# Kernel tuning notes

Hardware: AMD Instinct MI355X
Metric: run time of the kernel (lower is better)

The kernel has to match this reference:

```python
import jax, jax.numpy as jnp
import numpy as np

B, P, D, F = 2048, 16, 1024, 512  # batch, n_prompt, dim, fusion_dim
S = 2 * P  # sequence length
H = D // 2  # classifier hidden
LN_EPS = 1e-5


def _ln_relu(y, g, b):
    mu = jnp.mean(y, axis=-1, keepdims=True)
    var = jnp.mean(jnp.square(y - mu), axis=-1, keepdims=True)
    return jax.nn.relu((y - mu) * jax.lax.rsqrt(var + LN_EPS) * g + b)


def setup_inputs() -> dict:
    key = jax.random.key(0)
    ks = jax.random.split(key, 24)
    n = lambda k, shp, scale: jax.random.normal(k, shp, dtype=jnp.float32) * scale
    return {
        "q": n(ks[0], (B, S, D), 1.0),
        # nn.MultiheadAttention (1 head, batch_first)
        "in_proj_w": n(ks[1], (3 * D, D), 1.0 / np.sqrt(D)),
        "in_proj_b": jnp.zeros((3 * D,), jnp.float32),
        "out_w": n(ks[2], (D, D), 1.0 / np.sqrt(D)),
        "out_b": jnp.zeros((D,), jnp.float32),
        # 32 per-position classifiers, stacked: Linear(D,H)+ReLU+Linear(H,1)+ReLU
        "cls_w1": n(ks[3], (S, H, D), 1.0 / np.sqrt(D)),
        "cls_b1": jnp.zeros((S, H), jnp.float32),
        "cls_w2": n(ks[4], (S, H), 1.0 / np.sqrt(H)),
        "cls_b2": jnp.zeros((S,), jnp.float32),
        # fusion / projector heads: Linear(D,F)+LayerNorm(F)+ReLU
        "fus_w": n(ks[5], (F, D), 1.0 / np.sqrt(D)),
        "fus_b": jnp.zeros((F,), jnp.float32),
        "fus_g": jnp.ones((F,), jnp.float32),
        "fus_be": jnp.zeros((F,), jnp.float32),
        "pa_w": n(ks[6], (F, D), 1.0 / np.sqrt(D)),
        "pa_b": jnp.zeros((F,), jnp.float32),
        "pa_g": jnp.ones((F,), jnp.float32),
        "pa_be": jnp.zeros((F,), jnp.float32),
        "pv_w": n(ks[7], (F, D), 1.0 / np.sqrt(D)),
        "pv_b": jnp.zeros((F,), jnp.float32),
        "pv_g": jnp.ones((F,), jnp.float32),
        "pv_be": jnp.zeros((F,), jnp.float32),
    }


def reference(q, in_proj_w, in_proj_b, out_w, out_b,
              cls_w1, cls_b1, cls_w2, cls_b2,
              fus_w, fus_b, fus_g, fus_be,
              pa_w, pa_b, pa_g, pa_be,
              pv_w, pv_b, pv_g, pv_be):
    # --- single-head self-attention (nn.MultiheadAttention, eval mode) ---
    wq, wk, wv = jnp.split(in_proj_w, 3, axis=0)
    bq, bk, bv = jnp.split(in_proj_b, 3, axis=0)
    qp = jnp.einsum('bsd,ed->bse', q, wq) + bq
    kp = jnp.einsum('bsd,ed->bse', q, wk) + bk
    vp = jnp.einsum('bsd,ed->bse', q, wv) + bv
    scores = jnp.einsum('bse,bte->bst', qp, kp) / jnp.sqrt(jnp.float32(D))
    attn = jax.nn.softmax(scores, axis=-1)
    q_att = jnp.einsum('bst,bte->bse', attn, vp)
    q_att = jnp.einsum('bse,de->bsd', q_att, out_w) + out_b

    # --- per-position tiny classifiers, batched over the 32 slots ---
    h = jax.nn.relu(jnp.einsum('bsd,shd->bsh', q, cls_w1) + cls_b1)  # [B,S,H]
    d = jax.nn.relu(jnp.einsum('bsh,sh->bs', h, cls_w2) + cls_b2)    # [B,S]

    d_a = jax.nn.softmax(d[:, :P], axis=-1)
    d_v = jax.nn.softmax(d[:, P:], axis=-1)
    audio = jnp.einsum('bsd,bs->bd', q_att[:, :P, :], d_a)
    video = jnp.einsum('bsd,bs->bd', q_att[:, P:, :], d_v)
    fusion = (audio + video) * 0.5

    fusion_h = _ln_relu(fusion @ fus_w.T + fus_b, fus_g, fus_be)
    fusion_a = _ln_relu(audio @ pa_w.T + pa_b, pa_g, pa_be)
    fusion_v = _ln_relu(video @ pv_w.T + pv_b, pv_g, pv_be)
    return (fusion_h, fusion_a, fusion_v, d_a, d_v)
```

## Files before the change

### kernel.cpp

```cpp
#include <hip/hip_runtime.h>

#define Bdim 2048
#define Sdim 32
#define Ddim 1024
#define Fdim 512
#define Hdim 512

typedef __bf16 bf16_t;
typedef __bf16 bf16x8 __attribute__((ext_vector_type(8)));
typedef __bf16 bf16x4 __attribute__((ext_vector_type(4)));
typedef float  f32x4  __attribute__((ext_vector_type(4)));

#define BM 128
#define BN 128
#define BK 32

__device__ __forceinline__ void gll16(const bf16_t* g, bf16_t* l) {
  __builtin_amdgcn_global_load_lds((const __attribute__((address_space(1))) void*)g,
                                   (__attribute__((address_space(3))) void*)l,
                                   16, 0, 0);
}

__device__ __forceinline__ int swz32(int row, int k) {
  return row * 32 + (((((k >> 3) ^ ((row >> 1) & 3))) << 3) | (k & 7));
}

__global__ void k_cvt_all(const float* __restrict__ q, const float* __restrict__ ipw,
                          const float* __restrict__ ow, const float* __restrict__ cw1,
                          const float* __restrict__ fusw, const float* __restrict__ paw,
                          const float* __restrict__ pvw,
                          bf16_t* __restrict__ q16, bf16_t* __restrict__ w16,
                          bf16_t* __restrict__ ow16, bf16_t* __restrict__ cls16,
                          bf16_t* __restrict__ hw16) {
  long v = (long)blockIdx.x * 256 + threadIdx.x;
  const float* s; bf16_t* d; long off;
  if (v < 16777216L)      { s = q;    d = q16;            off = 0; }
  else if (v < 17563648L) { s = ipw;  d = w16;            off = 16777216L; }
  else if (v < 17825792L) { s = ow;   d = ow16;           off = 17563648L; }
  else if (v < 22020096L) { s = cw1;  d = cls16;          off = 17825792L; }
  else if (v < 22151168L) { s = fusw; d = hw16;           off = 22020096L; }
  else if (v < 22282240L) { s = paw;  d = hw16 + 524288;  off = 22151168L; }
  else                    { s = pvw;  d = hw16 + 1048576; off = 22282240L; }
  long i = (v - off) * 4;
  float4 t = *(const float4*)(s + i);
  bf16x4 o;
  o[0] = (bf16_t)t.x; o[1] = (bf16_t)t.y; o[2] = (bf16_t)t.z; o[3] = (bf16_t)t.w;
  *(bf16x4*)(d + i) = o;
}

__global__ void k_bias_pre(const float* __restrict__ ipw, const float* __restrict__ ipb,
                           const float* __restrict__ ow, const float* __restrict__ ob,
                           float* __restrict__ u, float* __restrict__ w,
                           float* __restrict__ bp, float* __restrict__ c0) {
  int blk = blockIdx.x, tid = threadIdx.x;
  if (blk < 4) {
    int d = blk * 256 + tid;
    float acc = 0.f;
    #pragma unroll 8
    for (int e = 0; e < Ddim; ++e) acc += ipw[(long)e * Ddim + d] * ipb[Ddim + e];
    u[d] = acc;
  } else if (blk < 8) {
    int d = (blk - 4) * 256 + tid;
    float acc = 0.f;
    #pragma unroll 8
    for (int e = 0; e < Ddim; ++e) acc += ipw[(long)(Ddim + e) * Ddim + d] * ipb[e];
    w[d] = acc;
  } else if (blk < 136) {
    int o = (blk - 8) * 8 + (tid >> 5);
    int l = tid & 31;
    float acc = 0.f;
    #pragma unroll 4
    for (int e = l; e < Ddim; e += 32) acc += ow[(long)o * Ddim + e] * ipb[2 * Ddim + e];
    #pragma unroll
    for (int m = 1; m < 32; m <<= 1) acc += __shfl_xor(acc, m);
    if (l == 0) bp[o] = acc + ob[o];
  } else {
    __shared__ float red[256];
    float acc = 0.f;
    for (int e = tid; e < Ddim; e += 256) acc += ipb[e] * ipb[Ddim + e];
    red[tid] = acc;
    __syncthreads();
    for (int off = 128; off; off >>= 1) {
      if (tid < off) red[tid] += red[tid + off];
      __syncthreads();
    }
    if (tid == 0) c0[0] = red[0];
  }
}

template<int AT, int BT>
__device__ __forceinline__ void gemm_tile(const bf16_t* __restrict__ A, long lda,
                                          const bf16_t* __restrict__ Bt, long ldb,
                                          long m0, long n0, int K,
                                          bf16_t* sa, bf16_t* sb, f32x4 acc[4][4]) {
  const int tid  = threadIdx.x;
  const int wave = tid >> 6;
  const int lane = tid & 63;
  const int quad = lane >> 4;
  const int l16  = lane & 15;
  const int wm = (wave & 1) * 64;
  const int wn = (wave >> 1) * 64;

  for (int kt = 0; kt < K; kt += BK) {
    __syncthreads();
    if constexpr (AT == 0) {
      #pragma unroll
      for (int r = 0; r < 2; ++r) {
        int L = r * 256 + tid;
        int row = L >> 2, cs = L & 3;
        int csrc = cs ^ ((row >> 1) & 3);
        gll16(A + (m0 + row) * lda + kt + csrc * 8, sa + (long)(r * 256 + wave * 64) * 8);
      }
    } else {
      #pragma unroll
      for (int r = 0; r < 2; ++r) {
        int L = r * 256 + tid;
        int gk = L >> 4, gm = (L & 15) * 8;
        bf16x8 v = *(const bf16x8*)(A + (long)(kt + gk) * lda + m0 + gm);
        #pragma unroll
        for (int j = 0; j < 8; ++j) sa[swz32(gm + j, gk)] = v[j];
      }
    }
    if constexpr (BT == 0) {
      #pragma unroll
      for (int r = 0; r < 2; ++r) {
        int L = r * 256 + tid;
        int row = L >> 2, cs = L & 3;
        int csrc = cs ^ ((row >> 1) & 3);
        gll16(Bt + (n0 + row) * ldb + kt + csrc * 8, sb + (long)(r * 256 + wave * 64) * 8);
      }
    } else {
      #pragma unroll
      for (int r = 0; r < 2; ++r) {
        int L = r * 256 + tid;
        int gk = L >> 4, gn = (L & 15) * 8;
        bf16x8 v = *(const bf16x8*)(Bt + (long)(kt + gk) * ldb + n0 + gn);
        #pragma unroll
        for (int j = 0; j < 8; ++j) sb[swz32(gn + j, gk)] = v[j];
      }
    }
    __syncthreads();
    bf16x8 af[4], bfr[4];
    #pragma unroll
    for (int i = 0; i < 4; ++i) {
      int row = wm + i * 16 + l16;
      af[i] = *(const bf16x8*)(sa + row * 32 + ((quad ^ ((row >> 1) & 3)) << 3));
    }
    #pragma unroll
    for (int j = 0; j < 4; ++j) {
      int row = wn + j * 16 + l16;
      bfr[j] = *(const bf16x8*)(sb + row * 32 + ((quad ^ ((row >> 1) & 3)) << 3));
    }
    #pragma unroll
    for (int i = 0; i < 4; ++i)
      #pragma unroll
      for (int j = 0; j < 4; ++j)
        acc[i][j] = __builtin_amdgcn_mfma_f32_16x16x32_bf16(bfr[j], af[i], acc[i][j], 0, 0, 0);
  }
}

template<int AT, int BT>
__global__ __launch_bounds__(256) void k_gemm_bf16(
    const bf16_t* __restrict__ A, long lda, long sAz,
    const bf16_t* __restrict__ Bt, long ldb, long sBz,
    bf16_t* __restrict__ C, long ldc, long sCz,
    const float* __restrict__ bias, int K) {
  __shared__ bf16_t sa[BM * BK];
  __shared__ bf16_t sb[BN * BK];
  long n0 = (long)blockIdx.x * BN;
  long m0 = (long)blockIdx.y * BM;
  long z  = blockIdx.z;
  const bf16_t* Az = A + z * sAz;
  const bf16_t* Bz = Bt + z * sBz;
  bf16_t* Cz = C + z * sCz;
  f32x4 acc[4][4];
  #pragma unroll
  for (int i = 0; i < 4; ++i)
    #pragma unroll
    for (int j = 0; j < 4; ++j) acc[i][j] = (f32x4){0.f, 0.f, 0.f, 0.f};
  gemm_tile<AT, BT>(Az, lda, Bz, ldb, m0, n0, K, sa, sb, acc);
  const int tid = threadIdx.x, wave = tid >> 6, lane = tid & 63;
  const int quad = lane >> 4, l16 = lane & 15;
  const int wm = (wave & 1) * 64, wn = (wave >> 1) * 64;
  #pragma unroll
  for (int i = 0; i < 4; ++i) {
    long row = m0 + wm + i * 16 + l16;
    #pragma unroll
    for (int j = 0; j < 4; ++j) {
      long col = n0 + wn + j * 16 + quad * 4;
      f32x4 b4 = bias ? *(const f32x4*)(bias + col) : (f32x4){0.f, 0.f, 0.f, 0.f};
      bf16x4 o;
      #pragma unroll
      for (int r = 0; r < 4; ++r) o[r] = (bf16_t)(acc[i][j][r] + b4[r]);
      *(bf16x4*)(Cz + row * ldc + col) = o;
    }
  }
}

__global__ __launch_bounds__(256) void k_gemm_f32(
    const bf16_t* __restrict__ A, long lda, long sAz,
    const bf16_t* __restrict__ Bt, long ldb, long sBz,
    float* __restrict__ C, long ldc, long sCz, int K) {
  __shared__ bf16_t sa[BM * BK];
  __shared__ bf16_t sb[BN * BK];
  long n0 = (long)blockIdx.x * BN;
  long m0 = (long)blockIdx.y * BM;
  long z  = blockIdx.z;
  const bf16_t* Az = A + z * sAz;
  const bf16_t* Bz = Bt + z * sBz;
  float* Cz = C + z * sCz;
  f32x4 acc[4][4];
  #pragma unroll
  for (int i = 0; i < 4; ++i)
    #pragma unroll
    for (int j = 0; j < 4; ++j) acc[i][j] = (f32x4){0.f, 0.f, 0.f, 0.f};
  gemm_tile<0, 0>(Az, lda, Bz, ldb, m0, n0, K, sa, sb, acc);
  const int tid = threadIdx.x, wave = tid >> 6, lane = tid & 63;
  const int quad = lane >> 4, l16 = lane & 15;
  const int wm = (wave & 1) * 64, wn = (wave >> 1) * 64;
  #pragma unroll
  for (int i = 0; i < 4; ++i) {
    long row = m0 + wm + i * 16 + l16;
    #pragma unroll
    for (int j = 0; j < 4; ++j) {
      long col = n0 + wn + j * 16 + quad * 4;
      *(f32x4*)(Cz + row * ldc + col) = acc[i][j];
    }
  }
}

__global__ __launch_bounds__(512, 2) void k_gemm_big8(
    const bf16_t* __restrict__ A, const bf16_t* __restrict__ Bt,
    bf16_t* __restrict__ C) {
  __shared__ bf16_t sa[2][256 * 64];
  __shared__ bf16_t sb[2][256 * 64];
  const int tid = threadIdx.x, wave = tid >> 6, lane = tid & 63;
  const int quad = lane >> 4, l16 = lane & 15;
  int lin = blockIdx.x;
  int c = lin & 7, t0 = lin >> 3;
  int wg = c * 128 + t0;
  long m0 = (long)(wg >> 2) * 256;
  long n0 = (long)(wg & 3) * 256;
  const int wm = (wave >> 2) * 128;
  const int wn = (wave & 3) * 64;

  const int csA = tid & 7;
  const bf16_t* aSrc = A + (m0 + (tid >> 3)) * 1024 + (long)((csA ^ ((tid >> 4) & 7)) * 8);
  const int t2 = tid & 255;
  const bf16_t* bSrc = Bt + (n0 + (t2 >> 3)) * 1024 + (long)(((t2 & 7) ^ ((t2 >> 4) & 7)) * 8);

  const int swzk0 = ((0 * 4 + quad) ^ (l16 >> 1)) << 3;
  const int swzk1 = ((1 * 4 + quad) ^ (l16 >> 1)) << 3;
  const int aBase = (wm + l16) * 64;
  const int bBase = (wn + l16) * 64;

  f32x4 acc[8][4];
  #pragma unroll
  for (int i = 0; i < 8; ++i)
    #pragma unroll
    for (int j = 0; j < 4; ++j) acc[i][j] = (f32x4){0.f, 0.f, 0.f, 0.f};

  bf16x8 afc[8], bfr0[4], bfr1[4];

#define ST_AQ(SB, KT, Q) \
  gll16(aSrc + (long)(Q) * 65536 + (KT), &sa[SB][(Q) * 4096 + wave * 512])
#define ST_BP(SB, KT, OA, OB) do {                                             \
    int oct_ = (wave < 4) ? (OA) : (OB);                                       \
    gll16(bSrc + (long)oct_ * 32768 + (KT),                                    \
          &sb[SB][oct_ * 2048 + (wave & 3) * 512]);                            \
  } while (0)

#define LD_AF(CB, MH) do {                                                     \
    _Pragma("unroll")                                                          \
    for (int i = 0; i < 4; ++i) {                                              \
      afc[i * 2 + 0] = *(const bf16x8*)(&sa[CB][aBase + (MH) * 4096 + i * 1024 + swzk0]); \
      afc[i * 2 + 1] = *(const bf16x8*)(&sa[CB][aBase + (MH) * 4096 + i * 1024 + swzk1]); \
    } } while (0)
#define LD_BF(CB, NH, DST) do {                                                \
    _Pragma("unroll")                                                          \
    for (int jj = 0; jj < 2; ++jj) {                                           \
      DST[jj * 2 + 0] = *(const bf16x8*)(&sb[CB][bBase + (NH) * 2048 + jj * 1024 + swzk0]); \
      DST[jj * 2 + 1] = *(const bf16x8*)(&sb[CB][bBase + (NH) * 2048 + jj * 1024 + swzk1]); \
    } } while (0)

#define MFMA16(BF, IOFF, JOFF) do {                                            \
    __builtin_amdgcn_s_setprio(1);                                             \
    _Pragma("unroll")                                                          \
    for (int i = 0; i < 4; ++i)                                                \
      _Pragma("unroll")                                                        \
      for (int jj = 0; jj < 2; ++jj)                                           \
        _Pragma("unroll")                                                      \
        for (int kh = 0; kh < 2; ++kh)                                         \
          acc[(IOFF) + i][(JOFF) + jj] = __builtin_amdgcn_mfma_f32_16x16x32_bf16( \
              BF[jj * 2 + kh], afc[i * 2 + kh], acc[(IOFF) + i][(JOFF) + jj], 0, 0, 0); \
    __builtin_amdgcn_s_setprio(0);                                             \
    __builtin_amdgcn_sched_barrier(0);                                         \
  } while (0)

#define BAR1() do {                                                            \
    asm volatile("" ::: "memory");                                             \
    __builtin_amdgcn_s_barrier();                                              \
    asm volatile("s_waitcnt lgkmcnt(0)" ::: "memory");                         \
    __builtin_amdgcn_sched_barrier(0);                                         \
  } while (0)
#define BAR2V() do {                                                           \
    asm volatile("s_waitcnt vmcnt(4)" ::: "memory");                           \
    __builtin_amdgcn_s_barrier();                                              \
    asm volatile("" ::: "memory");                                             \
  } while (0)
#define BAR2() do {                                                            \
    asm volatile("" ::: "memory");                                             \
    __builtin_amdgcn_s_barrier();                                              \
    asm volatile("" ::: "memory");                                             \
  } while (0)

#define TILE(CB, SB, KT2) do {                                                 \
                                                    \
    LD_AF(CB, 0); LD_BF(CB, 0, bfr0);                                          \
    ST_AQ(SB, KT2, 0); ST_AQ(SB, KT2, 2);                                      \
    BAR1(); MFMA16(bfr0, 0, 0); BAR2V();                                       \
                                                    \
    LD_BF(CB, 1, bfr1);                                                        \
    ST_BP(SB, KT2, 0, 4); ST_BP(SB, KT2, 2, 6);                                \
    BAR1(); MFMA16(bfr1, 0, 2); BAR2V();                                       \
                                                    \
    LD_AF(CB, 1);                                                              \
    ST_BP(SB, KT2, 1, 5); ST_BP(SB, KT2, 3, 7);                                \
    BAR1(); MFMA16(bfr1, 4, 2); BAR2();                                        \
              \
    ST_AQ(SB, KT2, 1); ST_AQ(SB, KT2, 3);                                      \
    BAR1(); MFMA16(bfr0, 4, 0); BAR2V();                                       \
  } while (0)

  ST_AQ(0, 0, 0); ST_AQ(0, 0, 2);
  ST_BP(0, 0, 0, 4); ST_BP(0, 0, 2, 6);
  ST_BP(0, 0, 1, 5); ST_BP(0, 0, 3, 7);
  ST_AQ(0, 0, 1); ST_AQ(0, 0, 3);
  BAR2V();

  #pragma unroll 1
  for (int x = 0; x < 16; x += 2) {
    int ktA = (x + 1) * 64;
    int ktB = (x + 2) * 64;
    TILE(0, 1, ktA);
    TILE(1, 0, ktB);
  }

#undef ST_AQ
#undef ST_BP
#undef LD_AF
#undef LD_BF
#undef MFMA16
#undef BAR1
#undef BAR2V
#undef BAR2
#undef TILE

  #pragma unroll
  for (int i = 0; i < 8; ++i) {
    long row = m0 + wm + i * 16 + l16;
    #pragma unroll
    for (int j = 0; j < 4; ++j) {
      long col = n0 + wn + j * 16 + quad * 4;
      bf16x4 o;
      #pragma unroll
      for (int r = 0; r < 4; ++r) o[r] = (bf16_t)(acc[i][j][r]);
      *(bf16x4*)(C + row * 1024 + col) = o;
    }
  }
}

__global__ __launch_bounds__(256) void k_gemm_cls(
    const bf16_t* __restrict__ q16, const bf16_t* __restrict__ w1,
    const float* __restrict__ b1, const float* __restrict__ w2,
    float* __restrict__ dsum) {
  __shared__ bf16_t sa[BM * BK];
  __shared__ bf16_t sb[BN * BK];
  int lin = ((int)blockIdx.z * 16 + blockIdx.y) * 4 + blockIdx.x;
  int c = lin & 7, j0 = lin >> 3;
  int p = c + 8 * (j0 >> 2);
  long n0 = (long)(j0 & 3) * BN;
  int s = p >> 4;
  long m0 = (long)(p & 15) * BM;
  const bf16_t* A  = q16 + (long)s * Ddim;
  const bf16_t* Bt = w1 + (long)s * Hdim * Ddim;
  f32x4 acc[4][4];
  #pragma unroll
  for (int i = 0; i < 4; ++i)
    #pragma unroll
    for (int j = 0; j < 4; ++j) acc[i][j] = (f32x4){0.f, 0.f, 0.f, 0.f};
  gemm_tile<0, 0>(A, (long)Sdim * Ddim, Bt, Ddim, m0, n0, Ddim, sa, sb, acc);
  const int tid = threadIdx.x, wave = tid >> 6, lane = tid & 63;
  const int quad = lane >> 4, l16 = lane & 15;
  const int wm = (wave & 1) * 64, wn = (wave >> 1) * 64;
  const float* b1s = b1 + (long)s * Hdim;
  const float* w2s = w2 + (long)s * Hdim;
  #pragma unroll
  for (int i = 0; i < 4; ++i) {
    float vsum = 0.f;
    #pragma unroll
    for (int j = 0; j < 4; ++j) {
      long col = n0 + wn + j * 16 + quad * 4;
      f32x4 b4 = *(const f32x4*)(b1s + col);
      f32x4 w4 = *(const f32x4*)(w2s + col);
      #pragma unroll
      for (int r = 0; r < 4; ++r)
        vsum += fmaxf(acc[i][j][r] + b4[r], 0.f) * w4[r];
    }
    vsum += __shfl_xor(vsum, 16);
    vsum += __shfl_xor(vsum, 32);
    if (lane < 16) {
      long row = m0 + wm + i * 16 + l16;
      atomicAdd(&dsum[row * Sdim + s], vsum);
    }
  }
}

__global__ void k_finalize_d(const float* __restrict__ dsum, const float* __restrict__ cb2,
                             float* __restrict__ daws, float* __restrict__ out_da,
                             float* __restrict__ out_dv) {
  int t = blockIdx.x * 256 + threadIdx.x;
  int b = t >> 5, s = t & 31;
  float v = fmaxf(dsum[t] + cb2[s], 0.f);
  float m = v;
  #pragma unroll
  for (int mask = 1; mask < 16; mask <<= 1) m = fmaxf(m, __shfl_xor(m, mask));
  float e = __expf(v - m);
  float sum = e;
  #pragma unroll
  for (int mask = 1; mask < 16; mask <<= 1) sum += __shfl_xor(sum, mask);
  float r = e / sum;
  daws[t] = r;
  if (s < 16) out_da[b * 16 + s] = r;
  else        out_dv[b * 16 + (s - 16)] = r;
}

#define QPAD 264
__global__ __launch_bounds__(256) void k_attn_pool(
    const bf16_t* __restrict__ q16, const bf16_t* __restrict__ G16,
    const float* __restrict__ daws, const float* __restrict__ u,
    const float* __restrict__ wv, const float* __restrict__ c0p,
    bf16_t* __restrict__ pooled) {
  __shared__ bf16_t qc[32 * QPAD];
  __shared__ bf16_t gc[32 * QPAD];
  __shared__ float sc[32][33];
  __shared__ float qup[32][8], qwp[32][8];
  __shared__ float quL[32], qwL[32], caL[32], cvL[32], daL[16], dvL[16];
  const int tid = threadIdx.x, wave = tid >> 6, lane = tid & 63;
  const int quad = lane >> 4, l16 = lane & 15;
  const long b = blockIdx.x;
  const bf16_t* qb = q16 + b * (Sdim * Ddim);
  const bf16_t* gb = G16 + b * (Sdim * Ddim);
  if (tid < 32) {
    float dval = daws[b * Sdim + tid];
    if (tid < 16) daL[tid] = dval; else dvL[tid - 16] = dval;
  }
  qup[tid >> 3][tid & 7] = 0.f;
  qwp[tid >> 3][tid & 7] = 0.f;
  const int ti = wave & 1, tj = wave >> 1;
  f32x4 acc = (f32x4){0.f, 0.f, 0.f, 0.f};
  for (int kc = 0; kc < Ddim; kc += 256) {
    __syncthreads();
    #pragma unroll
    for (int r = 0; r < 4; ++r) {
      int L = r * 256 + tid;
      int row = L >> 5, koff = (L & 31) * 8;
      *(bf16x8*)(qc + row * QPAD + koff) = *(const bf16x8*)(qb + (long)row * Ddim + kc + koff);
      *(bf16x8*)(gc + row * QPAD + koff) = *(const bf16x8*)(gb + (long)row * Ddim + kc + koff);
    }
    __syncthreads();
    #pragma unroll
    for (int kk = 0; kk < 8; ++kk) {
      bf16x8 a  = *(const bf16x8*)(gc + (ti * 16 + l16) * QPAD + kk * 32 + quad * 8);
      bf16x8 bb = *(const bf16x8*)(qc + (tj * 16 + l16) * QPAD + kk * 32 + quad * 8);
      acc = __builtin_amdgcn_mfma_f32_16x16x32_bf16(a, bb, acc, 0, 0, 0);
    }
    {
      int s2 = tid & 31, sl = tid >> 5;
      float pu = 0.f, pw = 0.f;
      const bf16_t* qrow = qc + s2 * QPAD + sl * 32;
      const float* ub = u + kc + sl * 32;
      const float* wb = wv + kc + sl * 32;
      #pragma unroll
      for (int kb = 0; kb < 4; ++kb) {
        bf16x8 qv = *(const bf16x8*)(qrow + kb * 8);
        f32x4 u0 = *(const f32x4*)(ub + kb * 8);
        f32x4 u1 = *(const f32x4*)(ub + kb * 8 + 4);
        f32x4 w0 = *(const f32x4*)(wb + kb * 8);
        f32x4 w1 = *(const f32x4*)(wb + kb * 8 + 4);
        #pragma unroll
        for (int e = 0; e < 4; ++e) {
          pu += (float)qv[e] * u0[e] + (float)qv[e + 4] * u1[e];
          pw += (float)qv[e] * w0[e] + (float)qv[e + 4] * w1[e];
        }
      }
      qup[s2][sl] += pu;
      qwp[s2][sl] += pw;
    }
  }
  __syncthreads();
  if (tid < 32) {
    float a0 = 0.f, a1 = 0.f;
    for (int k = 0; k < 8; ++k) { a0 += qup[tid][k]; a1 += qwp[tid][k]; }
    quL[tid] = a0; qwL[tid] = a1;
  }
  __syncthreads();
  {
    float c00 = c0p[0];
    int col = tj * 16 + l16;
    #pragma unroll
    for (int r = 0; r < 4; ++r) {
      int row = ti * 16 + quad * 4 + r;
      sc[row][col] = (acc[r] + quL[row] + qwL[col] + c00) * 0.03125f;
    }
  }
  __syncthreads();
  if (tid < 32) {
    float mx = -1e30f;
    for (int t = 0; t < 32; ++t) mx = fmaxf(mx, sc[tid][t]);
    float sum = 0.f;
    for (int t = 0; t < 32; ++t) { float e = __expf(sc[tid][t] - mx); sc[tid][t] = e; sum += e; }
    float inv = 1.f / sum;
    for (int t = 0; t < 32; ++t) sc[tid][t] *= inv;
  }
  __syncthreads();
  if (tid < 32) {
    float a0 = 0.f, a1 = 0.f;
    for (int s2 = 0; s2 < 16; ++s2) a0 += daL[s2] * sc[s2][tid];
    for (int s2 = 0; s2 < 16; ++s2) a1 += dvL[s2] * sc[16 + s2][tid];
    caL[tid] = a0; cvL[tid] = a1;
  }
  __syncthreads();
  {
    int d0 = tid * 4;
    float ap[4] = {0.f, 0.f, 0.f, 0.f}, vp[4] = {0.f, 0.f, 0.f, 0.f};
    for (int t = 0; t < 32; ++t) {
      float ca = caL[t], cv = cvL[t];
      bf16x4 qv = *(const bf16x4*)(qb + (long)t * Ddim + d0);
      #pragma unroll
      for (int e = 0; e < 4; ++e) {
        float x = (float)qv[e];
        ap[e] += ca * x;
        vp[e] += cv * x;
      }
    }
    bf16x4 pf, pa, pv;
    #pragma unroll
    for (int e = 0; e < 4; ++e) {
      pf[e] = (bf16_t)(0.5f * (ap[e] + vp[e]));
      pa[e] = (bf16_t)ap[e];
      pv[e] = (bf16_t)vp[e];
    }
    *(bf16x4*)(pooled + b * 3072 + d0)        = pf;
    *(bf16x4*)(pooled + b * 3072 + 1024 + d0) = pa;
    *(bf16x4*)(pooled + b * 3072 + 2048 + d0) = pv;
  }
}

__global__ __launch_bounds__(256) void k_ln(
    const float* __restrict__ Y,
    const float* __restrict__ fb, const float* __restrict__ fg, const float* __restrict__ fbe,
    const float* __restrict__ ab, const float* __restrict__ ag, const float* __restrict__ abe,
    const float* __restrict__ vb, const float* __restrict__ vg, const float* __restrict__ vbe,
    float* __restrict__ out) {
  int wave = threadIdx.x >> 6, lane = threadIdx.x & 63;
  long row = (long)blockIdx.x * 4 + wave;
  int head = (int)(row >> 11);
  const float* bb = (head == 0) ? fb : (head == 1) ? ab : vb;
  const float* gg = (head == 0) ? fg : (head == 1) ? ag : vg;
  const float* be = (head == 0) ? fbe : (head == 1) ? abe : vbe;
  const float* y = Y + row * Fdim + lane * 8;
  float v[8];
  float s = 0.f;
  #pragma unroll
  for (int k = 0; k < 8; ++k) { v[k] = y[k] + bb[lane * 8 + k]; s += v[k]; }
  #pragma unroll
  for (int m = 1; m < 64; m <<= 1) s += __shfl_xor(s, m);
  float mu = s * (1.f / Fdim);
  float vs = 0.f;
  #pragma unroll
  for (int k = 0; k < 8; ++k) { float t = v[k] - mu; vs += t * t; }
  #pragma unroll
  for (int m = 1; m < 64; m <<= 1) vs += __shfl_xor(vs, m);
  float inv = rsqrtf(vs * (1.f / Fdim) + 1e-5f);
  float* o = out + row * Fdim + lane * 8;
  #pragma unroll
  for (int k = 0; k < 8; ++k) {
    float t = (v[k] - mu) * inv * gg[lane * 8 + k] + be[lane * 8 + k];
    o[k] = fmaxf(t, 0.f);
  }
}

extern "C" void kernel_launch(void* const* d_in, const int* in_sizes, int n_in,
                              void* d_out, int out_size, void* d_ws, size_t ws_size,
                              hipStream_t stream) {
  const float* q    = (const float*)d_in[0];
  const float* ipw  = (const float*)d_in[1];
  const float* ipb  = (const float*)d_in[2];
  const float* ow   = (const float*)d_in[3];
  const float* ob   = (const float*)d_in[4];
  const float* cw1  = (const float*)d_in[5];
  const float* cb1  = (const float*)d_in[6];
  const float* cw2  = (const float*)d_in[7];
  const float* cb2  = (const float*)d_in[8];
  const float* fusw = (const float*)d_in[9];
  const float* fusb = (const float*)d_in[10];
  const float* fusg = (const float*)d_in[11];
  const float* fusbe= (const float*)d_in[12];
  const float* paw  = (const float*)d_in[13];
  const float* pab  = (const float*)d_in[14];
  const float* pag  = (const float*)d_in[15];
  const float* pabe = (const float*)d_in[16];
  const float* pvw  = (const float*)d_in[17];
  const float* pvb  = (const float*)d_in[18];
  const float* pvg  = (const float*)d_in[19];
  const float* pvbe = (const float*)d_in[20];
  float* out = (float*)d_out;

  const size_t o_q16   = 0;
  const size_t o_w16   = 134217728;
  const size_t o_ow16  = 140509184;
  const size_t o_cls16 = 142606336;
  const size_t o_hw16  = 176160768;
  const size_t o_Mt    = 179306496;
  const size_t o_Nt    = 181403648;
  const size_t o_G16   = 183500800;
  const size_t o_pool  = 317718528;
  const size_t o_u     = 330301440;
  const size_t o_wv    = 330305536;
  const size_t o_bp    = 330309632;
  const size_t o_c0    = 330313728;
  const size_t o_dsum  = 330313984;
  const size_t o_daws  = 330576128;
  const size_t total   = 330838272;
  if (ws_size < total) return;

  char* ws = (char*)d_ws;
  bf16_t* q16   = (bf16_t*)(ws + o_q16);
  bf16_t* w16   = (bf16_t*)(ws + o_w16);
  bf16_t* Wq16  = w16;
  bf16_t* Wk16  = w16 + 1048576;
  bf16_t* Wv16  = w16 + 2097152;
  bf16_t* ow16  = (bf16_t*)(ws + o_ow16);
  bf16_t* cls16 = (bf16_t*)(ws + o_cls16);
  bf16_t* hw16  = (bf16_t*)(ws + o_hw16);
  bf16_t* Mt    = (bf16_t*)(ws + o_Mt);
  bf16_t* Nt    = (bf16_t*)(ws + o_Nt);
  bf16_t* G16   = (bf16_t*)(ws + o_G16);
  bf16_t* S116  = (bf16_t*)(ws + o_G16);
  float*  Yf    = (float*)(ws + o_G16 + 12582912);
  bf16_t* pool16= (bf16_t*)(ws + o_pool);
  float*  uf    = (float*)(ws + o_u);
  float*  wvf   = (float*)(ws + o_wv);
  float*  bpf   = (float*)(ws + o_bp);
  float*  c0f   = (float*)(ws + o_c0);
  float*  dsum  = (float*)(ws + o_dsum);
  float*  daws  = (float*)(ws + o_daws);

  k_cvt_all<<<dim3(87552), dim3(256), 0, stream>>>(
      q, ipw, ow, cw1, fusw, paw, pvw, q16, w16, ow16, cls16, hw16);

  k_bias_pre<<<dim3(137), dim3(256), 0, stream>>>(ipw, ipb, ow, ob, uf, wvf, bpf, c0f);

  k_gemm_bf16<1, 1><<<dim3(8, 8, 1), dim3(256), 0, stream>>>(
      Wk16, Ddim, 0, Wq16, Ddim, 0, Mt, Ddim, 0, nullptr, Ddim);

  k_gemm_bf16<0, 1><<<dim3(8, 8, 1), dim3(256), 0, stream>>>(
      ow16, Ddim, 0, Wv16, Ddim, 0, Nt, Ddim, 0, nullptr, Ddim);

  k_gemm_big8<<<dim3(1024), dim3(512), 0, stream>>>(q16, Mt, G16);

  hipMemsetAsync(dsum, 0, (size_t)Bdim * Sdim * sizeof(float), stream);
  k_gemm_cls<<<dim3(4, 16, 32), dim3(256), 0, stream>>>(q16, cls16, cb1, cw2, dsum);

  k_finalize_d<<<dim3(256), dim3(256), 0, stream>>>(
      dsum, cb2, daws, out + 3145728, out + 3145728 + 32768);

  k_attn_pool<<<dim3(2048), dim3(256), 0, stream>>>(q16, G16, daws, uf, wvf, c0f, pool16);

  k_gemm_bf16<0, 0><<<dim3(8, 48, 1), dim3(256), 0, stream>>>(
      pool16, Ddim, 0, Nt, Ddim, 0, S116, Ddim, 0, bpf, Ddim);

  k_gemm_f32<<<dim3(4, 16, 3), dim3(256), 0, stream>>>(
      S116, 3L * Ddim, Ddim, hw16, Ddim, (long)Fdim * Ddim,
      Yf, Fdim, (long)Bdim * Fdim, Ddim);

  k_ln<<<dim3(1536), dim3(256), 0, stream>>>(
      Yf, fusb, fusg, fusbe, pab, pag, pabe, pvb, pvg, pvbe, out);
}
```

Measured before the change: 1.033 ms.

## Restructure big GEMM pipeline with ping-pong waves and split LDS halves

Rewrites the main 65536x1024x1024 bf16 GEMM kernel's software pipeline. LDS is reorganized into four 128-row quarter buffers per stage, and waves are staggered so half issue LDS reads before MFMAs and half after. Fragment loads for the next tile are prefetched into double-buffered register sets, which replaces the per-phase sched barriers with fewer combined waitcnt+barrier syncs. The goal is better overlap of LDS reads, global-to-LDS loads and MFMA work, at the cost of more registers and more complex hazard ordering.

```diff
diff --git a/kernel.cpp b/kernel.cpp
--- a/kernel.cpp
+++ b/kernel.cpp
@@ -229,30 +229,34 @@
   }
 }
 
-__global__ __launch_bounds__(512, 2) void k_gemm_big8(
+__global__ __launch_bounds__(512, 2) void k_gemm_bigR(
     const bf16_t* __restrict__ A, const bf16_t* __restrict__ Bt,
     bf16_t* __restrict__ C) {
-  __shared__ bf16_t sa[2][256 * 64];
-  __shared__ bf16_t sb[2][256 * 64];
+  __shared__ bf16_t L[2][4][8192];
   const int tid = threadIdx.x, wave = tid >> 6, lane = tid & 63;
   const int quad = lane >> 4, l16 = lane & 15;
   int lin = blockIdx.x;
-  int c = lin & 7, t0 = lin >> 3;
-  int wg = c * 128 + t0;
+  int cx = lin & 7, t0 = lin >> 3;
+  int wg = cx * 128 + t0;
   long m0 = (long)(wg >> 2) * 256;
   long n0 = (long)(wg & 3) * 256;
-  const int wm = (wave >> 2) * 128;
+  const int hA = wave >> 2;
+  const int hB = (wave & 3) >> 1;
+  const int wm = hA * 128;
   const int wn = (wave & 3) * 64;
-
-  const int csA = tid & 7;
-  const bf16_t* aSrc = A + (m0 + (tid >> 3)) * 1024 + (long)((csA ^ ((tid >> 4) & 7)) * 8);
-  const int t2 = tid & 255;
-  const bf16_t* bSrc = Bt + (n0 + (t2 >> 3)) * 1024 + (long)(((t2 & 7) ^ ((t2 >> 4) & 7)) * 8);
-
+  const int bq = (wave & 1) * 64;
+  const int sA4 = wave & 3;
+  const int sB4 = ((wave & 1) << 1) | hA;
+  const int tA = sA4 * 64 + lane;
+  const bf16_t* aStage = A + (m0 + hA * 128 + (tA >> 3)) * 1024L
+                           + (long)(((tA & 7) ^ ((tA >> 4) & 7)) * 8);
+  const int tB = sB4 * 64 + lane;
+  const bf16_t* bStage = Bt + (n0 + hB * 128 + (tB >> 3)) * 1024L
+                            + (long)(((tB & 7) ^ ((tB >> 4) & 7)) * 8);
+  const int aDstO = sA4 * 512;
+  const int bDstO = sB4 * 512;
   const int swzk0 = ((0 * 4 + quad) ^ (l16 >> 1)) << 3;
   const int swzk1 = ((1 * 4 + quad) ^ (l16 >> 1)) << 3;
-  const int aBase = (wm + l16) * 64;
-  const int bBase = (wn + l16) * 64;
 
   f32x4 acc[8][4];
   #pragma unroll
@@ -260,30 +264,27 @@
     #pragma unroll
     for (int j = 0; j < 4; ++j) acc[i][j] = (f32x4){0.f, 0.f, 0.f, 0.f};
 
-  bf16x8 afc[8], bfr0[4], bfr1[4];
-
-#define ST_AQ(SB, KT, Q) \
-  gll16(aSrc + (long)(Q) * 65536 + (KT), &sa[SB][(Q) * 4096 + wave * 512])
-#define ST_BP(SB, KT, OA, OB) do {                                             \
-    int oct_ = (wave < 4) ? (OA) : (OB);                                       \
-    gll16(bSrc + (long)oct_ * 32768 + (KT),                                    \
-          &sb[SB][oct_ * 2048 + (wave & 3) * 512]);                            \
-  } while (0)
-
-#define LD_AF(CB, MH) do {                                                     \
+  bf16x8 A0f[8], A1f[8], B0f[4], B1f[4];
+
+#define STA(D, KT, LL) gll16(aStage + (long)(KT) + (LL) * 32768L, &L[D][hA][aDstO + (LL) * 2048])
+#define STB(D, KT, LL) gll16(bStage + (long)(KT) + (LL) * 32768L, &L[D][2 + hB][bDstO + (LL) * 2048])
+
+#define RDA(DST, D, MQ) do {                                                   \
     _Pragma("unroll")                                                          \
     for (int i = 0; i < 4; ++i) {                                              \
-      afc[i * 2 + 0] = *(const bf16x8*)(&sa[CB][aBase + (MH) * 4096 + i * 1024 + swzk0]); \
-      afc[i * 2 + 1] = *(const bf16x8*)(&sa[CB][aBase + (MH) * 4096 + i * 1024 + swzk1]); \
+      int ro = ((MQ) * 64 + i * 16 + l16) * 64;                                \
+      DST[i * 2 + 0] = *(const bf16x8*)(&L[D][hA][ro + swzk0]);                \
+      DST[i * 2 + 1] = *(const bf16x8*)(&L[D][hA][ro + swzk1]);                \
     } } while (0)
-#define LD_BF(CB, NH, DST) do {                                                \
+#define RDB(DST, D, NQ) do {                                                   \
     _Pragma("unroll")                                                          \
     for (int jj = 0; jj < 2; ++jj) {                                           \
-      DST[jj * 2 + 0] = *(const bf16x8*)(&sb[CB][bBase + (NH) * 2048 + jj * 1024 + swzk0]); \
-      DST[jj * 2 + 1] = *(const bf16x8*)(&sb[CB][bBase + (NH) * 2048 + jj * 1024 + swzk1]); \
+      int ro = (bq + (NQ) * 32 + jj * 16 + l16) * 64;                          \
+      DST[jj * 2 + 0] = *(const bf16x8*)(&L[D][2 + hB][ro + swzk0]);           \
+      DST[jj * 2 + 1] = *(const bf16x8*)(&L[D][2 + hB][ro + swzk1]);           \
     } } while (0)
 
-#define MFMA16(BF, IOFF, JOFF) do {                                            \
+#define MF(AF, BF, MQ, NQ) do {                                                \
     __builtin_amdgcn_s_setprio(1);                                             \
     _Pragma("unroll")                                                          \
     for (int i = 0; i < 4; ++i)                                                \
@@ -291,69 +292,74 @@
       for (int jj = 0; jj < 2; ++jj)                                           \
         _Pragma("unroll")                                                      \
         for (int kh = 0; kh < 2; ++kh)                                         \
-          acc[(IOFF) + i][(JOFF) + jj] = __builtin_amdgcn_mfma_f32_16x16x32_bf16( \
-              BF[jj * 2 + kh], afc[i * 2 + kh], acc[(IOFF) + i][(JOFF) + jj], 0, 0, 0); \
+          acc[(MQ) * 4 + i][(NQ) * 2 + jj] = __builtin_amdgcn_mfma_f32_16x16x32_bf16( \
+              BF[jj * 2 + kh], AF[i * 2 + kh], acc[(MQ) * 4 + i][(NQ) * 2 + jj], 0, 0, 0); \
     __builtin_amdgcn_s_setprio(0);                                             \
-    __builtin_amdgcn_sched_barrier(0);                                         \
   } while (0)
 
-#define BAR1() do {                                                            \
-    asm volatile("" ::: "memory");                                             \
-    __builtin_amdgcn_s_barrier();                                              \
+#define SYNCL() do {                                                           \
     asm volatile("s_waitcnt lgkmcnt(0)" ::: "memory");                         \
-    __builtin_amdgcn_sched_barrier(0);                                         \
-  } while (0)
-#define BAR2V() do {                                                           \
-    asm volatile("s_waitcnt vmcnt(4)" ::: "memory");                           \
     __builtin_amdgcn_s_barrier();                                              \
     asm volatile("" ::: "memory");                                             \
   } while (0)
-#define BAR2() do {                                                            \
-    asm volatile("" ::: "memory");                                             \
+#define SYNCV(VM) do {                                                         \
+    asm volatile("s_waitcnt vmcnt(" #VM ") lgkmcnt(0)" ::: "memory");          \
     __builtin_amdgcn_s_barrier();                                              \
     asm volatile("" ::: "memory");                                             \
   } while (0)
 
-#define TILE(CB, SB, KT2) do {                                                 \
-                                                    \
-    LD_AF(CB, 0); LD_BF(CB, 0, bfr0);                                          \
-    ST_AQ(SB, KT2, 0); ST_AQ(SB, KT2, 2);                                      \
-    BAR1(); MFMA16(bfr0, 0, 0); BAR2V();                                       \
-                                                    \
-    LD_BF(CB, 1, bfr1);                                                        \
-    ST_BP(SB, KT2, 0, 4); ST_BP(SB, KT2, 2, 6);                                \
-    BAR1(); MFMA16(bfr1, 0, 2); BAR2V();                                       \
-                                                    \
-    LD_AF(CB, 1);                                                              \
-    ST_BP(SB, KT2, 1, 5); ST_BP(SB, KT2, 3, 7);                                \
-    BAR1(); MFMA16(bfr1, 4, 2); BAR2();                                        \
-              \
-    ST_AQ(SB, KT2, 1); ST_AQ(SB, KT2, 3);                                      \
-    BAR1(); MFMA16(bfr0, 4, 0); BAR2V();                                       \
+#define TILE(CUR, NXT, KTN, KTNN, NOTLAST) do {                                \
+                               \
+    if (wave & 4) { RDB(B1f, CUR, 1); MF(A0f, B0f, 0, 0); }                    \
+    else          { MF(A0f, B0f, 0, 0); RDB(B1f, CUR, 1); }                    \
+    STA(NXT, KTN, 2); STA(NXT, KTN, 3);                                        \
+    SYNCL();                                                                   \
+                       \
+    if (wave & 4) { RDA(A1f, CUR, 1); MF(A0f, B1f, 0, 1); }                    \
+    else          { MF(A0f, B1f, 0, 1); RDA(A1f, CUR, 1); }                    \
+    STB(NXT, KTN, 1); STB(NXT, KTN, 3);                                        \
+    SYNCV(6);                                                                  \
+                       \
+    if (NOTLAST) {                                                             \
+      if (wave & 4) { RDA(A0f, NXT, 0); MF(A1f, B1f, 1, 1); }                  \
+      else          { MF(A1f, B1f, 1, 1); RDA(A0f, NXT, 0); }                  \
+    } else { MF(A1f, B1f, 1, 1); }                                             \
+    STA(CUR, KTNN, 0); STA(CUR, KTNN, 1);                                      \
+    SYNCV(6);                                                                  \
+          \
+    MF(A1f, B0f, 1, 0);                                                        \
+    if (NOTLAST) { RDB(B0f, NXT, 0); }                                         \
+    STB(CUR, KTNN, 0); STB(CUR, KTNN, 2);                                      \
+    SYNCV(4);                                                                  \
   } while (0)
 
-  ST_AQ(0, 0, 0); ST_AQ(0, 0, 2);
-  ST_BP(0, 0, 0, 4); ST_BP(0, 0, 2, 6);
-  ST_BP(0, 0, 1, 5); ST_BP(0, 0, 3, 7);
-  ST_AQ(0, 0, 1); ST_AQ(0, 0, 3);
-  BAR2V();
+  STA(0, 0, 0);  STA(0, 0, 1);
+  STB(0, 0, 0);  STB(0, 0, 2);
+  STA(0, 0, 2);  STA(0, 0, 3);
+  STB(0, 0, 1);  STB(0, 0, 3);
+  STA(1, 64, 0); STA(1, 64, 1);
+  STB(1, 64, 0); STB(1, 64, 2);
+  asm volatile("s_waitcnt vmcnt(8)" ::: "memory");
+  __builtin_amdgcn_s_barrier();
+  asm volatile("" ::: "memory");
+  RDA(A0f, 0, 0);
+  RDB(B0f, 0, 0);
+  SYNCV(4);
 
   #pragma unroll 1
-  for (int x = 0; x < 16; x += 2) {
-    int ktA = (x + 1) * 64;
-    int ktB = (x + 2) * 64;
-    TILE(0, 1, ktA);
-    TILE(1, 0, ktB);
-  }
-
-#undef ST_AQ
-#undef ST_BP
-#undef LD_AF
-#undef LD_BF
-#undef MFMA16
-#undef BAR1
-#undef BAR2V
-#undef BAR2
+  for (int xx = 0; xx < 8; ++xx) {
+    int X = 2 * xx;
+    TILE(0, 1, (X + 1) * 64, (X + 2) * 64, true);
+    TILE(1, 0, (X + 2) * 64, (X + 3) * 64, (xx < 7));
+  }
+
+#undef STA
+#undef STB
+#undef RDA
+#undef RDB
+#undef MF
+#undef SYNCL
+#undef SYNCV
 #undef TILE
 
   #pragma unroll
@@ -668,7 +674,7 @@
   k_gemm_bf16<0, 1><<<dim3(8, 8, 1), dim3(256), 0, stream>>>(
       ow16, Ddim, 0, Wv16, Ddim, 0, Nt, Ddim, 0, nullptr, Ddim);
 
-  k_gemm_big8<<<dim3(1024), dim3(512), 0, stream>>>(q16, Mt, G16);
+  k_gemm_bigR<<<dim3(1024), dim3(512), 0, stream>>>(q16, Mt, G16);
 
   hipMemsetAsync(dsum, 0, (size_t)Bdim * Sdim * sizeof(float), stream);
   k_gemm_cls<<<dim3(4, 16, 32), dim3(256), 0, stream>>>(q16, cls16, cb1, cw2, dsum);
```

Result: slower. 1.529 ms (+48.0%).
